# Optimization experiments

Hardware: AMD Instinct MI355X
Metric: run time of the kernel (lower is better)

Reference implementation:

```python
import jax, jax.numpy as jnp
import numpy as np
import math

B, L, D_MODEL, D_HEAD = 4, 4096, 1024, 128

def setup_inputs() -> dict:
    key = jax.random.key(0)
    ks = jax.random.split(key, 9)
    s = 0.02
    return {
        "inp_q": jax.random.normal(ks[0], (B, L, D_MODEL), jnp.float32),
        "inp_k": jax.random.normal(ks[1], (B, L, D_MODEL), jnp.float32),
        "inp_v": jax.random.normal(ks[2], (B, L, D_MODEL), jnp.float32),
        "Wq": jax.random.normal(ks[3], (D_HEAD, D_MODEL), jnp.float32) * s,
        "bq": jax.random.normal(ks[4], (D_HEAD,), jnp.float32) * s,
        "Wk": jax.random.normal(ks[5], (D_HEAD, D_MODEL), jnp.float32) * s,
        "bk": jax.random.normal(ks[6], (D_HEAD,), jnp.float32) * s,
        "Wv": jax.random.normal(ks[7], (D_HEAD, D_MODEL), jnp.float32) * s,
        "bv": jax.random.normal(ks[8], (D_HEAD,), jnp.float32) * s,
    }

def reference(inp_q, inp_k, inp_v, Wq, bq, Wk, bk, Wv, bv):
    d_q = Wq.shape[0]
    # torch nn.Linear: y = x @ W.T + b
    Q = jnp.einsum('bld,qd->blq', inp_q, Wq) + bq   # [B, L, d_q]
    K = jnp.einsum('bld,kd->blk', inp_k, Wk) + bk   # [B, L, d_k]
    V = jnp.einsum('bld,vd->blv', inp_v, Wv) + bv   # [B, L, d_v]
    scores = jnp.einsum('bqe,bke->bqk', Q, K) / math.sqrt(d_q)  # [B, Lq, Lk]
    # NOTE: original uses nn.Softmax(dim=1) -> normalizes over the QUERY axis
    S = jax.nn.softmax(scores, axis=1)
    H = jnp.einsum('bqk,bkv->bqv', S, V)            # [B, Lq, d_v]
    return H
```

## Files before the change

### kernel.cpp

```cpp
#include <hip/hip_runtime.h>
#include <hip/hip_bf16.h>

#define B_  4
#define L_  4096
#define DM  1024
#define DH  128
#define KS  4
#define QS  4

#define SC2 0.12752844f

typedef __bf16 bf16_t;
typedef __attribute__((ext_vector_type(8))) __bf16 bf16x8;
typedef __attribute__((ext_vector_type(4))) __bf16 bf16x4;
typedef __attribute__((ext_vector_type(4))) float f32x4;

#if __has_builtin(__builtin_amdgcn_exp2f)
#define EXP2F(x) __builtin_amdgcn_exp2f(x)
#else
#define EXP2F(x) exp2f(x)
#endif

__device__ __forceinline__ f32x4 mfma16(bf16x8 a, bf16x8 b, f32x4 c) {
    return __builtin_amdgcn_mfma_f32_16x16x32_bf16(a, b, c, 0, 0, 0);
}

__device__ __forceinline__ int swz(int row, int rowbytes, int colbyte) {
    int slot = colbyte >> 4;
    return row * rowbytes + (((slot ^ (row & 7)) << 4) | (colbyte & 15));
}

__device__ __forceinline__ void gload_lds16(const void* g, void* l) {
    __builtin_amdgcn_global_load_lds((const __attribute__((address_space(1))) void*)g,
                                     (__attribute__((address_space(3))) void*)l, 16, 0, 0);
}

__global__ __launch_bounds__(256) void wcvt_kernel(
    const float* __restrict__ Wq, const float* __restrict__ Wk, const float* __restrict__ Wv,
    bf16_t* __restrict__ Wb)
{
    int idx = (blockIdx.x * 256 + threadIdx.x) * 8;
    int which = idx >> 17;
    int rem = idx & 131071;
    const float* W = which == 0 ? Wq : (which == 1 ? Wk : Wv);
    float4 a = *(const float4*)&W[rem];
    float4 b = *(const float4*)&W[rem + 4];
    bf16x8 o;
    o[0] = (__bf16)a.x; o[1] = (__bf16)a.y; o[2] = (__bf16)a.z; o[3] = (__bf16)a.w;
    o[4] = (__bf16)b.x; o[5] = (__bf16)b.y; o[6] = (__bf16)b.z; o[7] = (__bf16)b.w;
    *(bf16x8*)&Wb[idx] = o;
}

__global__ __launch_bounds__(256) void proj_kernel(
    const float* __restrict__ Xq, const float* __restrict__ Xk, const float* __restrict__ Xv,
    const bf16_t* __restrict__ Wb,
    const float* __restrict__ bq, const float* __restrict__ bk, const float* __restrict__ bv,
    bf16_t* __restrict__ Q, bf16_t* __restrict__ K, bf16_t* __restrict__ V)
{
    const int which = blockIdx.y;
    const float* X    = which == 0 ? Xq : (which == 1 ? Xk : Xv);
    const float* bias = which == 0 ? bq : (which == 1 ? bk : bv);
    bf16_t*      O    = which == 0 ? Q  : (which == 1 ? K  : V);
    const bf16_t* Wm  = Wb + (size_t)which * DH * DM;

    __shared__ float  Xlds[64 * 64];
    __shared__ bf16_t Wlds[128 * 64];

    const int tid  = threadIdx.x;
    const int lane = tid & 63;
    const int wave = tid >> 6;
    const int wm = wave >> 1, wn = wave & 1;
    const int row0 = blockIdx.x * 64;

    f32x4 acc[2][4] = {};

    for (int kk = 0; kk < DM; kk += 64) {
        __syncthreads();
        #pragma unroll
        for (int j = 0; j < 4; ++j) {
            int c = wave * 4 + j;
            int r = c * 4 + (lane >> 4);
            int s = lane & 15;
            gload_lds16(&X[(size_t)(row0 + r) * DM + kk + ((s ^ (r & 7)) << 2)],
                        (char*)Xlds + c * 1024);
        }
        #pragma unroll
        for (int j = 0; j < 4; ++j) {
            int c = wave * 4 + j;
            int r = c * 8 + (lane >> 3);
            int s = lane & 7;
            gload_lds16(&Wm[(size_t)r * DM + kk + ((s ^ (r & 7)) << 3)],
                        (char*)Wlds + c * 1024);
        }
        __syncthreads();
        #pragma unroll
        for (int ks = 0; ks < 2; ++ks) {
            bf16x8 af[2], bfr[4];
            #pragma unroll
            for (int mi = 0; mi < 2; ++mi) {
                int r = wm * 32 + mi * 16 + (lane & 15);
                int rx = r & 7;
                int s0 = ks * 8 + (lane >> 4) * 2;
                float4 x0 = *(const float4*)&Xlds[r * 64 + ((s0 ^ rx) << 2)];
                float4 x1 = *(const float4*)&Xlds[r * 64 + (((s0 + 1) ^ rx) << 2)];
                bf16x8 a;
                a[0] = (__bf16)x0.x; a[1] = (__bf16)x0.y; a[2] = (__bf16)x0.z; a[3] = (__bf16)x0.w;
                a[4] = (__bf16)x1.x; a[5] = (__bf16)x1.y; a[6] = (__bf16)x1.z; a[7] = (__bf16)x1.w;
                af[mi] = a;
            }
            #pragma unroll
            for (int ni = 0; ni < 4; ++ni) {
                int r = wn * 64 + ni * 16 + (lane & 15);
                int t = ks * 4 + (lane >> 4);
                bfr[ni] = *(const bf16x8*)((const char*)Wlds + r * 128 + ((t ^ (r & 7)) << 4));
            }
            #pragma unroll
            for (int mi = 0; mi < 2; ++mi)
                #pragma unroll
                for (int ni = 0; ni < 4; ++ni)
                    acc[mi][ni] = mfma16(af[mi], bfr[ni], acc[mi][ni]);
        }
    }
    #pragma unroll
    for (int ni = 0; ni < 4; ++ni) {
        int h = wn * 64 + ni * 16 + (lane & 15);
        float bb = bias[h];
        #pragma unroll
        for (int mi = 0; mi < 2; ++mi)
            #pragma unroll
            for (int j = 0; j < 4; ++j) {
                int r = row0 + wm * 32 + mi * 16 + (lane >> 4) * 4 + j;
                O[(size_t)r * DH + h] = (__bf16)(acc[mi][ni][j] + bb);
            }
    }
}

__global__ __launch_bounds__(256) void stats_kernel(
    const bf16_t* __restrict__ Q, const bf16_t* __restrict__ K,
    float* __restrict__ Mpart, float* __restrict__ Lpart)
{
    const int b  = blockIdx.y;
    const int k0 = blockIdx.x * 64;
    const int qs = blockIdx.z;
    const int tid = threadIdx.x, lane = tid & 63, wave = tid >> 6;

    __shared__ bf16_t Klds[64 * 128];
    __shared__ bf16_t Qlds[128 * 128];

    const bf16_t* Kb = K + ((size_t)b * L_ + k0) * DH;
    #pragma unroll
    for (int it = 0; it < 4; ++it) {
        int id = it * 256 + tid;
        int r = id >> 4, s = id & 15;
        bf16x8 x = *(const bf16x8*)&Kb[(size_t)r * DH + s * 8];
        *(bf16x8*)((char*)Klds + swz(r, 256, s * 16)) = x;
    }
    __syncthreads();
    bf16x8 kfr[4][4];
    #pragma unroll
    for (int ni = 0; ni < 4; ++ni)
        #pragma unroll
        for (int ds = 0; ds < 4; ++ds) {
            int r = ni * 16 + (lane & 15);
            kfr[ni][ds] = *(const bf16x8*)((const char*)Klds + swz(r, 256, ds * 64 + (lane >> 4) * 16));
        }

    float mrun[4], lrun[4];
    #pragma unroll
    for (int ni = 0; ni < 4; ++ni) { mrun[ni] = -1e30f; lrun[ni] = 0.f; }

    const bf16_t* Qb = Q + (size_t)b * L_ * DH;
    const int qbase = qs * (L_ / QS);
    for (int q0 = qbase; q0 < qbase + L_ / QS; q0 += 128) {
        __syncthreads();
        #pragma unroll
        for (int it = 0; it < 8; ++it) {
            int id = it * 256 + tid;
            int r = id >> 4, s = id & 15;
            bf16x8 x = *(const bf16x8*)&Qb[(size_t)(q0 + r) * DH + s * 8];
            *(bf16x8*)((char*)Qlds + swz(r, 256, s * 16)) = x;
        }
        __syncthreads();
        f32x4 st[2][4] = {};
        #pragma unroll
        for (int mi = 0; mi < 2; ++mi)
            #pragma unroll
            for (int ds = 0; ds < 4; ++ds) {
                int r = wave * 32 + mi * 16 + (lane & 15);
                bf16x8 af = *(const bf16x8*)((const char*)Qlds + swz(r, 256, ds * 64 + (lane >> 4) * 16));
                #pragma unroll
                for (int ni = 0; ni < 4; ++ni)
                    st[mi][ni] = mfma16(af, kfr[ni][ds], st[mi][ni]);
            }
        #pragma unroll
        for (int ni = 0; ni < 4; ++ni) {
            float cm = -1e30f;
            #pragma unroll
            for (int mi = 0; mi < 2; ++mi)
                #pragma unroll
                for (int j = 0; j < 4; ++j) cm = fmaxf(cm, st[mi][ni][j]);
            cm *= SC2;
            cm = fmaxf(cm, __shfl_xor(cm, 16, 64));
            cm = fmaxf(cm, __shfl_xor(cm, 32, 64));
            float mnew = fmaxf(mrun[ni], cm);
            float p = 0.f;
            #pragma unroll
            for (int mi = 0; mi < 2; ++mi)
                #pragma unroll
                for (int j = 0; j < 4; ++j)
                    p += EXP2F(st[mi][ni][j] * SC2 - mnew);
            p += __shfl_xor(p, 16, 64);
            p += __shfl_xor(p, 32, 64);
            lrun[ni] = lrun[ni] * EXP2F(mrun[ni] - mnew) + p;
            mrun[ni] = mnew;
        }
    }
    __syncthreads();
    float* redm = (float*)Klds;
    float* redl = redm + 256;
    if (lane < 16) {
        #pragma unroll
        for (int ni = 0; ni < 4; ++ni) {
            redm[wave * 64 + ni * 16 + lane] = mrun[ni];
            redl[wave * 64 + ni * 16 + lane] = lrun[ni];
        }
    }
    __syncthreads();
    if (tid < 64) {
        float m0 = redm[tid], m1 = redm[64 + tid], m2v = redm[128 + tid], m3 = redm[192 + tid];
        float mt = fmaxf(fmaxf(m0, m1), fmaxf(m2v, m3));
        float lt = redl[tid]       * EXP2F(m0 - mt) + redl[64 + tid]  * EXP2F(m1 - mt)
                 + redl[128 + tid] * EXP2F(m2v - mt) + redl[192 + tid] * EXP2F(m3 - mt);
        Mpart[((size_t)qs * B_ + b) * L_ + k0 + tid] = mt;
        Lpart[((size_t)qs * B_ + b) * L_ + k0 + tid] = lt;
    }
}

__global__ __launch_bounds__(256) void comb_kernel(
    const float* __restrict__ Mpart, const float* __restrict__ Lpart,
    float* __restrict__ M2, float* __restrict__ Lsum)
{
    const size_t i = (size_t)blockIdx.x * 256 + threadIdx.x;
    const size_t N = (size_t)B_ * L_;
    float m = -1e30f;
    #pragma unroll
    for (int qs = 0; qs < QS; ++qs) m = fmaxf(m, Mpart[qs * N + i]);
    float l = 0.f;
    #pragma unroll
    for (int qs = 0; qs < QS; ++qs) l += Lpart[qs * N + i] * EXP2F(Mpart[qs * N + i] - m);
    M2[i] = m;
    Lsum[i] = l;
}

__global__ __launch_bounds__(256) void vt_kernel(
    const bf16_t* __restrict__ V, const float* __restrict__ Lsum, bf16_t* __restrict__ VT)
{
    const int b = blockIdx.z, v0 = blockIdx.y * 64, k0 = blockIdx.x * 64;
    __shared__ bf16_t tile[64][72];
    const int tid = threadIdx.x;
    const bf16_t* Vb = V + ((size_t)b * L_ + k0) * DH + v0;
    #pragma unroll
    for (int it = 0; it < 2; ++it) {
        int id = it * 256 + tid;
        int r = id >> 3, s = id & 7;
        bf16x8 x = *(const bf16x8*)&Vb[(size_t)r * DH + s * 8];
        *(bf16x8*)&tile[r][s * 8] = x;
    }
    __syncthreads();
    const int lane = tid & 63, wave = tid >> 6;
    float rl = 1.0f / Lsum[(size_t)b * L_ + k0 + lane];
    bf16_t* VTb = VT + ((size_t)b * DH + v0) * L_ + k0;
    #pragma unroll
    for (int i = 0; i < 16; ++i) {
        int v = wave * 16 + i;
        float x = (float)tile[lane][v];
        VTb[(size_t)v * L_ + lane] = (__bf16)(x * rl);
    }
}

__global__ __launch_bounds__(256) void pv_kernel(
    const bf16_t* __restrict__ Q, const bf16_t* __restrict__ K,
    const bf16_t* __restrict__ VT, const float* __restrict__ M2,
    float* __restrict__ out)
{
    const int b = blockIdx.y;
    const int q0 = blockIdx.x * 64;
    const int tid = threadIdx.x, lane = tid & 63, wave = tid >> 6;

    __shared__ bf16_t QPlds[64 * 128];
    __shared__ bf16_t Klds[64 * 128];
    __shared__ bf16_t VTlds[128 * 64];

    const bf16_t* Qb = Q + ((size_t)b * L_ + q0) * DH;
    #pragma unroll
    for (int it = 0; it < 4; ++it) {
        int id = it * 256 + tid;
        int r = id >> 4, s = id & 15;
        bf16x8 x = *(const bf16x8*)&Qb[(size_t)r * DH + s * 8];
        *(bf16x8*)((char*)QPlds + swz(r, 256, s * 16)) = x;
    }
    __syncthreads();
    bf16x8 qf[4][4];
    #pragma unroll
    for (int ni = 0; ni < 4; ++ni)
        #pragma unroll
        for (int ds = 0; ds < 4; ++ds) {
            int r = ni * 16 + (lane & 15);
            qf[ni][ds] = *(const bf16x8*)((const char*)QPlds + swz(r, 256, ds * 64 + (lane >> 4) * 16));
        }

    f32x4 acc[4][2] = {};
    const float*  m2b = M2 + (size_t)b * L_;
    const bf16_t* Kb  = K  + (size_t)b * L_ * DH;
    const bf16_t* VTb = VT + (size_t)b * DH * L_;
    bf16_t* Plds = QPlds;

    const int kbase = blockIdx.z * (L_ / KS);
    for (int kc = kbase; kc < kbase + L_ / KS; kc += 64) {
        __syncthreads();
        #pragma unroll
        for (int it = 0; it < 4; ++it) {
            int id = it * 256 + tid;
            int r = id >> 4, s = id & 15;
            bf16x8 x = *(const bf16x8*)&Kb[(size_t)(kc + r) * DH + s * 8];
            *(bf16x8*)((char*)Klds + swz(r, 256, s * 16)) = x;
        }
        #pragma unroll
        for (int it = 0; it < 4; ++it) {
            int id = it * 256 + tid;
            int r = id >> 3, s = id & 7;
            bf16x8 x = *(const bf16x8*)&VTb[(size_t)r * L_ + kc + s * 8];
            *(bf16x8*)((char*)VTlds + swz(r, 128, s * 16)) = x;
        }
        __syncthreads();
        f32x4 st[4] = {};
        #pragma unroll
        for (int ds = 0; ds < 4; ++ds) {
            int r = wave * 16 + (lane & 15);
            bf16x8 kf = *(const bf16x8*)((const char*)Klds + swz(r, 256, ds * 64 + (lane >> 4) * 16));
            #pragma unroll
            for (int ni = 0; ni < 4; ++ni)
                st[ni] = mfma16(kf, qf[ni][ds], st[ni]);
        }
        float4 mv = *(const float4*)&m2b[kc + wave * 16 + (lane >> 4) * 4];
        #pragma unroll
        for (int ni = 0; ni < 4; ++ni) {
            bf16x4 pk;
            pk[0] = (__bf16)EXP2F(st[ni][0] * SC2 - mv.x);
            pk[1] = (__bf16)EXP2F(st[ni][1] * SC2 - mv.y);
            pk[2] = (__bf16)EXP2F(st[ni][2] * SC2 - mv.z);
            pk[3] = (__bf16)EXP2F(st[ni][3] * SC2 - mv.w);
            int q = ni * 16 + (lane & 15);
            int colbyte = wave * 32 + (lane >> 4) * 8;
            *(bf16x4*)((char*)Plds + swz(q, 128, colbyte)) = pk;
        }
        __syncthreads();
        #pragma unroll
        for (int ks = 0; ks < 2; ++ks) {
            bf16x8 pf[4], vf[2];
            #pragma unroll
            for (int mi = 0; mi < 4; ++mi) {
                int q = mi * 16 + (lane & 15);
                pf[mi] = *(const bf16x8*)((const char*)Plds + swz(q, 128, ks * 64 + (lane >> 4) * 16));
            }
            #pragma unroll
            for (int ni = 0; ni < 2; ++ni) {
                int v = wave * 32 + ni * 16 + (lane & 15);
                vf[ni] = *(const bf16x8*)((const char*)VTlds + swz(v, 128, ks * 64 + (lane >> 4) * 16));
            }
            #pragma unroll
            for (int mi = 0; mi < 4; ++mi)
                #pragma unroll
                for (int ni = 0; ni < 2; ++ni)
                    acc[mi][ni] = mfma16(pf[mi], vf[ni], acc[mi][ni]);
        }
    }
    #pragma unroll
    for (int mi = 0; mi < 4; ++mi)
        #pragma unroll
        for (int ni = 0; ni < 2; ++ni)
            #pragma unroll
            for (int j = 0; j < 4; ++j) {
                int q = q0 + mi * 16 + (lane >> 4) * 4 + j;
                int v = wave * 32 + ni * 16 + (lane & 15);
                atomicAdd(&out[((size_t)b * L_ + q) * DH + v], acc[mi][ni][j]);
            }
}

extern "C" void kernel_launch(void* const* d_in, const int* in_sizes, int n_in,
                              void* d_out, int out_size, void* d_ws, size_t ws_size,
                              hipStream_t stream)
{
    const float* inq = (const float*)d_in[0];
    const float* ink = (const float*)d_in[1];
    const float* inv = (const float*)d_in[2];
    const float* Wq  = (const float*)d_in[3];
    const float* bq  = (const float*)d_in[4];
    const float* Wk  = (const float*)d_in[5];
    const float* bk  = (const float*)d_in[6];
    const float* Wv  = (const float*)d_in[7];
    const float* bv  = (const float*)d_in[8];
    float* out = (float*)d_out;

    const size_t nQKV = (size_t)B_ * L_ * DH;
    const size_t nBL  = (size_t)B_ * L_;
    char* ws = (char*)d_ws;
    bf16_t* Q  = (bf16_t*)ws;
    bf16_t* K  = Q + nQKV;
    bf16_t* V  = K + nQKV;
    bf16_t* VT = V + nQKV;
    float*  M2    = (float*)(VT + nQKV);
    float*  Lsum  = M2 + nBL;
    float*  Mpart = Lsum + nBL;
    float*  Lpart = Mpart + QS * nBL;
    bf16_t* Wbuf = VT;

    hipMemsetAsync(out, 0, nQKV * sizeof(float), stream);
    wcvt_kernel<<<dim3(192), 256, 0, stream>>>(Wq, Wk, Wv, Wbuf);
    proj_kernel<<<dim3(256, 3), 256, 0, stream>>>(inq, ink, inv, Wbuf, bq, bk, bv, Q, K, V);
    stats_kernel<<<dim3(L_ / 64, B_, QS), 256, 0, stream>>>(Q, K, Mpart, Lpart);
    comb_kernel<<<dim3(nBL / 256), 256, 0, stream>>>(Mpart, Lpart, M2, Lsum);
    vt_kernel<<<dim3(L_ / 64, DH / 64, B_), 256, 0, stream>>>(V, Lsum, VT);
    pv_kernel<<<dim3(L_ / 64, B_, KS), 256, 0, stream>>>(Q, K, VT, M2, out);
}
```

Measured before the change: 180.9 us.

## Convert X to bf16 at staging and double-buffer W tiles in projection

The projection kernel now loads X through registers, converts it to bf16 once, and stores 256-wide K chunks into a swizzled LDS buffer. This removes the per-MFMA float-to-bf16 conversion and halves the X LDS footprint per element. W tiles are double-buffered so the next 64-wide W slice is fetched asynchronously while the current one is consumed, with a vmcnt wait plus barrier per sub-step. The trade-offs are that X loads now go through VGPRs instead of direct-to-LDS, and the extra barriers add some synchronization cost.

```diff
diff --git a/kernel.cpp b/kernel.cpp
--- a/kernel.cpp
+++ b/kernel.cpp
@@ -51,6 +51,19 @@
     *(bf16x8*)&Wb[idx] = o;
 }
 
+__device__ __forceinline__ void stage_w(
+    const bf16_t* __restrict__ Wm, bf16_t* wb, int kt, int j, int lane, int wave)
+{
+    #pragma unroll
+    for (int jj = 0; jj < 4; ++jj) {
+        int c = wave * 4 + jj;
+        int r = c * 8 + (lane >> 3);
+        int s = lane & 7;
+        gload_lds16(&Wm[(size_t)r * DM + kt * 256 + j * 64 + ((s ^ (r & 7)) << 3)],
+                    (char*)wb + c * 1024);
+    }
+}
+
 __global__ __launch_bounds__(256) void proj_kernel(
     const float* __restrict__ Xq, const float* __restrict__ Xk, const float* __restrict__ Xv,
     const bf16_t* __restrict__ Wb,
@@ -63,73 +76,76 @@
     bf16_t*      O    = which == 0 ? Q  : (which == 1 ? K  : V);
     const bf16_t* Wm  = Wb + (size_t)which * DH * DM;
 
-    __shared__ float  Xlds[64 * 64];
-    __shared__ bf16_t Wlds[128 * 64];
+    __shared__ bf16_t Xlds[64 * 256];
+    __shared__ bf16_t Wlds[2][128 * 64];
 
     const int tid  = threadIdx.x;
     const int lane = tid & 63;
     const int wave = tid >> 6;
     const int wm = wave >> 1, wn = wave & 1;
+    const int i16 = lane & 15, g4 = lane >> 4;
+    const int l5  = lane >> 5, c32 = lane & 31;
     const int row0 = blockIdx.x * 64;
 
     f32x4 acc[2][4] = {};
 
-    for (int kk = 0; kk < DM; kk += 64) {
-        __syncthreads();
+    for (int kt = 0; kt < 4; ++kt) {
+        __syncthreads();
+        #pragma unroll
+        for (int p = 0; p < 8; ++p) {
+            int r = wave * 16 + p * 2 + l5;
+            const float* g = &X[(size_t)(row0 + r) * DM + kt * 256 + c32 * 8];
+            float4 a = *(const float4*)g;
+            float4 b = *(const float4*)(g + 4);
+            bf16x8 v;
+            v[0] = (__bf16)a.x; v[1] = (__bf16)a.y; v[2] = (__bf16)a.z; v[3] = (__bf16)a.w;
+            v[4] = (__bf16)b.x; v[5] = (__bf16)b.y; v[6] = (__bf16)b.z; v[7] = (__bf16)b.w;
+            *(bf16x8*)((char*)Xlds + r * 512 + ((c32 ^ (r & 7)) << 4)) = v;
+        }
+        stage_w(Wm, Wlds[0], kt, 0, lane, wave);
+        __syncthreads();
+
         #pragma unroll
         for (int j = 0; j < 4; ++j) {
-            int c = wave * 4 + j;
-            int r = c * 4 + (lane >> 4);
-            int s = lane & 15;
-            gload_lds16(&X[(size_t)(row0 + r) * DM + kk + ((s ^ (r & 7)) << 2)],
-                        (char*)Xlds + c * 1024);
-        }
-        #pragma unroll
-        for (int j = 0; j < 4; ++j) {
-            int c = wave * 4 + j;
-            int r = c * 8 + (lane >> 3);
-            int s = lane & 7;
-            gload_lds16(&Wm[(size_t)r * DM + kk + ((s ^ (r & 7)) << 3)],
-                        (char*)Wlds + c * 1024);
-        }
-        __syncthreads();
-        #pragma unroll
-        for (int ks = 0; ks < 2; ++ks) {
-            bf16x8 af[2], bfr[4];
-            #pragma unroll
-            for (int mi = 0; mi < 2; ++mi) {
-                int r = wm * 32 + mi * 16 + (lane & 15);
-                int rx = r & 7;
-                int s0 = ks * 8 + (lane >> 4) * 2;
-                float4 x0 = *(const float4*)&Xlds[r * 64 + ((s0 ^ rx) << 2)];
-                float4 x1 = *(const float4*)&Xlds[r * 64 + (((s0 + 1) ^ rx) << 2)];
-                bf16x8 a;
-                a[0] = (__bf16)x0.x; a[1] = (__bf16)x0.y; a[2] = (__bf16)x0.z; a[3] = (__bf16)x0.w;
-                a[4] = (__bf16)x1.x; a[5] = (__bf16)x1.y; a[6] = (__bf16)x1.z; a[7] = (__bf16)x1.w;
-                af[mi] = a;
-            }
-            #pragma unroll
-            for (int ni = 0; ni < 4; ++ni) {
-                int r = wn * 64 + ni * 16 + (lane & 15);
-                int t = ks * 4 + (lane >> 4);
-                bfr[ni] = *(const bf16x8*)((const char*)Wlds + r * 128 + ((t ^ (r & 7)) << 4));
-            }
-            #pragma unroll
-            for (int mi = 0; mi < 2; ++mi)
-                #pragma unroll
-                for (int ni = 0; ni < 4; ++ni)
-                    acc[mi][ni] = mfma16(af[mi], bfr[ni], acc[mi][ni]);
-        }
-    }
+            if (j < 3) stage_w(Wm, Wlds[(j + 1) & 1], kt, j + 1, lane, wave);
+            const bf16_t* wb = Wlds[j & 1];
+            #pragma unroll
+            for (int ks = 0; ks < 2; ++ks) {
+                int q = (j * 2 + ks) * 4 + g4;
+                bf16x8 af[2], bfr[4];
+                #pragma unroll
+                for (int mi = 0; mi < 2; ++mi) {
+                    int r = wm * 32 + mi * 16 + i16;
+                    af[mi] = *(const bf16x8*)((const char*)Xlds + r * 512 + ((q ^ (r & 7)) << 4));
+                }
+                #pragma unroll
+                for (int ni = 0; ni < 4; ++ni) {
+                    int rw = wn * 64 + ni * 16 + i16;
+                    int tt = ks * 4 + g4;
+                    bfr[ni] = *(const bf16x8*)((const char*)wb + rw * 128 + ((tt ^ (rw & 7)) << 4));
+                }
+                #pragma unroll
+                for (int mi = 0; mi < 2; ++mi)
+                    #pragma unroll
+                    for (int ni = 0; ni < 4; ++ni)
+                        acc[mi][ni] = mfma16(af[mi], bfr[ni], acc[mi][ni]);
+            }
+            if (j < 3) {
+                asm volatile("s_waitcnt vmcnt(0)" ::: "memory");
+                __builtin_amdgcn_s_barrier();
+            }
+        }
+    }
+
     #pragma unroll
     for (int ni = 0; ni < 4; ++ni) {
-        int h = wn * 64 + ni * 16 + (lane & 15);
+        int h = wn * 64 + ni * 16 + i16;
         float bb = bias[h];
         #pragma unroll
         for (int mi = 0; mi < 2; ++mi)
             #pragma unroll
             for (int j = 0; j < 4; ++j) {
-                int r = row0 + wm * 32 + mi * 16 + (lane >> 4) * 4 + j;
+                int r = row0 + wm * 32 + mi * 16 + g4 * 4 + j;
                 O[(size_t)r * DH + h] = (__bf16)(acc[mi][ni][j] + bb);
             }
     }
```

New measurement: 198.4 us. 9.7% more time.
